# Kernel tuning notes

Measured on AMD Instinct MI355X. Metric: run time of the kernel, lower is better.

Reference implementation:

```python
import jax, jax.numpy as jnp
import numpy as np

N = 50000
E = 800000
D_IN = 128
D_H = 128
N_CLASSES = 40
N_HIDDEN = 2


def _gcn_norm(edge_index, num_nodes):
    # Add self loops, compute symmetric normalization D^-1/2 (A+I) D^-1/2
    loops = jnp.arange(num_nodes, dtype=edge_index.dtype)
    src = jnp.concatenate([edge_index[0], loops])
    dst = jnp.concatenate([edge_index[1], loops])
    deg = jax.ops.segment_sum(jnp.ones_like(src, dtype=jnp.float32), dst,
                              num_segments=num_nodes)
    dinv = jnp.where(deg > 0, jax.lax.rsqrt(jnp.maximum(deg, 1.0)), 0.0)
    norm = dinv[src] * dinv[dst]  # [E+N]
    return src, dst, norm


def _gcn_conv(x, src, dst, norm, W, b):
    h = x @ W                          # [N, d_out] transform first (PyG order)
    msg = h[src] * norm[:, None]       # gather + scale, [E+N, d_out]
    out = jax.ops.segment_sum(msg, dst, num_segments=x.shape[0])
    return out + b


def setup_inputs() -> dict:
    key = jax.random.key(0)
    ks = jax.random.split(key, 8)
    x = jax.random.normal(ks[0], (N, D_IN), dtype=jnp.float32)
    edge_index = jax.random.randint(ks[1], (2, E), 0, N, dtype=jnp.int64)
    s = 1.0 / np.sqrt(D_IN)
    W1 = jax.random.uniform(ks[2], (D_IN, D_H), minval=-s, maxval=s, dtype=jnp.float32)
    b1 = jnp.zeros((D_H,), dtype=jnp.float32)
    sh = 1.0 / np.sqrt(D_H)
    Wh = jax.random.uniform(ks[3], (N_HIDDEN, D_H, D_H), minval=-sh, maxval=sh, dtype=jnp.float32)
    bh = jnp.zeros((N_HIDDEN, D_H), dtype=jnp.float32)
    Wf = jax.random.uniform(ks[4], (D_H, N_CLASSES), minval=-sh, maxval=sh, dtype=jnp.float32)
    bf = jnp.zeros((N_CLASSES,), dtype=jnp.float32)
    return {"x": x, "edge_index": edge_index, "W1": W1, "b1": b1,
            "Wh": Wh, "bh": bh, "Wf": Wf, "bf": bf}


def reference(x, edge_index, W1, b1, Wh, bh, Wf, bf):
    src, dst, norm = _gcn_norm(edge_index, x.shape[0])
    h = jax.nn.relu(_gcn_conv(x, src, dst, norm, W1, b1))
    for i in range(Wh.shape[0]):  # small fixed layer count
        h = jax.nn.relu(_gcn_conv(h, src, dst, norm, Wh[i], bh[i]))
    # extra relu in original forward is a no-op after relu above
    return h @ Wf + bf
```

## Files before the change

kernel.cpp:

```cpp
#include <hip/hip_runtime.h>

#define D 128
#define NC 40

typedef __attribute__((ext_vector_type(8))) short short8v;
typedef __attribute__((ext_vector_type(4))) float f32x4;

__device__ __forceinline__ unsigned short f2bf(float f) {
    unsigned u = __float_as_uint(f);
    u += 0x7fff + ((u >> 16) & 1);
    return (unsigned short)(u >> 16);
}
__device__ __forceinline__ float bf2f(unsigned short h) {
    return __uint_as_float(((unsigned)h) << 16);
}

__device__ __forceinline__ int load_idx(const int* ei, long long pos, int is64) {
    return is64 ? ei[pos * 2] : ei[pos];
}

__device__ __forceinline__ int detect64(const int* __restrict__ ei) {
    int lane = threadIdx.x & 63;
    int hi = ei[lane * 2 + 1];
    return __any(hi != 0) ? 0 : 1;
}


__global__ void count_convert_kernel(const int* __restrict__ ei, int* __restrict__ deg,
                                     int E, int EB,
                                     const float* __restrict__ W1, const float* __restrict__ Wh,
                                     const float* __restrict__ Wf,
                                     unsigned short* __restrict__ Wc1, unsigned short* __restrict__ Wch0,
                                     unsigned short* __restrict__ Wch1, unsigned short* __restrict__ Wcf) {
    if (blockIdx.x < EB) {
        int is64 = detect64(ei);
        int e = blockIdx.x * 256 + threadIdx.x;
        if (e < E) {
            int d = load_idx(ei, (long long)E + e, is64);
            atomicAdd(&deg[d], 1);
        }
    } else {
        int idx = (blockIdx.x - EB) * 256 + threadIdx.x;
        if (idx < 49152) {
            int which = idx >> 14;
            int j = idx & 16383;
            int nn = j >> 7, k = j & 127;
            const float* W = (which == 0) ? W1 : (which == 1) ? Wh : Wh + 16384;
            unsigned short* o = (which == 0) ? Wc1 : (which == 1) ? Wch0 : Wch1;
            float v = W[k * 128 + nn];
            unsigned short h = f2bf(v);
            o[j] = h;
            o[16384 + j] = f2bf(v - bf2f(h));
        } else if (idx < 49152 + 6144) {
            int j = idx - 49152;
            int nn = j >> 7, k = j & 127;
            float v = (nn < NC) ? Wf[k * NC + nn] : 0.f;
            unsigned short h = f2bf(v);
            Wcf[j] = h;
            Wcf[6144 + j] = f2bf(v - bf2f(h));
        }
    }
}

__global__ void scan1_kernel(const int* __restrict__ deg, int* __restrict__ bsum, int m) {
    int i = blockIdx.x * 512 + threadIdx.x;
    int v = (i < m) ? deg[i] : 0;
    #pragma unroll
    for (int off = 32; off; off >>= 1) v += __shfl_down(v, off, 64);
    __shared__ int ws[8];
    if ((threadIdx.x & 63) == 0) ws[threadIdx.x >> 6] = v;
    __syncthreads();
    if (threadIdx.x == 0) {
        int s = 0;
        #pragma unroll
        for (int j = 0; j < 8; ++j) s += ws[j];
        bsum[blockIdx.x] = s;
    }
}

__global__ void scan3_kernel(const int* __restrict__ deg, const int* __restrict__ bsum,
                             int* __restrict__ rowptr, int* __restrict__ fill,
                             float* __restrict__ dinv, int n, int E, int nb) {
    int t = threadIdx.x;
    int lane = t & 63, w = t >> 6;
    int pv = (t < nb && t < (int)blockIdx.x) ? bsum[t] : 0;
    int rs = pv;
    #pragma unroll
    for (int off = 32; off; off >>= 1) rs += __shfl_down(rs, off, 64);
    __shared__ int red[8];
    if (lane == 0) red[w] = rs;
    __syncthreads();
    int base = 0;
    #pragma unroll
    for (int j = 0; j < 8; ++j) base += red[j];
    __syncthreads();

    int i = blockIdx.x * 512 + t;
    int v = (i < n) ? deg[i] : 0;
    int s = v;
    #pragma unroll
    for (int off = 1; off < 64; off <<= 1) {
        int x = __shfl_up(s, off, 64);
        if (lane >= off) s += x;
    }
    __shared__ int wsum[8];
    if (lane == 63) wsum[w] = s;
    __syncthreads();
    int wbase = 0;
    #pragma unroll
    for (int j = 0; j < 8; ++j) if (j < w) wbase += wsum[j];
    int excl = base + wbase + s - v;
    if (i < n) {
        rowptr[i] = excl;
        fill[i]   = excl;
        dinv[i]   = rsqrtf((float)(v + 1));
    }
    if (i == 0) rowptr[n] = E;
}

__global__ void scatter_kernel(const int* __restrict__ ei, int* __restrict__ fill,
                               const float* __restrict__ dinv, int2* __restrict__ col2, int E) {
    int is64 = detect64(ei);
    int e = blockIdx.x * 256 + threadIdx.x;
    if (e >= E) return;
    int s = load_idx(ei, (long long)e, is64);
    int d = load_idx(ei, (long long)E + e, is64);
    int pos = atomicAdd(&fill[d], 1);
    col2[pos] = make_int2(s, __float_as_int(dinv[s]));
}

__launch_bounds__(512)
__global__ void fused_layer_kernel(const float4* __restrict__ h4,
                                   const unsigned short* __restrict__ Wcvt,
                                   const float* __restrict__ bias,
                                   const float* __restrict__ dinv,
                                   const int* __restrict__ rowptr, const int2* __restrict__ col2,
                                   float* __restrict__ out, int n) {
    __shared__ unsigned short Ah[16 * 128];
    __shared__ unsigned short Al[16 * 128];
    int t = threadIdx.x;
    int g = t >> 5, l = t & 31;
    int node = blockIdx.x * 16 + g;
    int nd = (node < n) ? node : (n - 1);
    float dn = dinv[nd];
    size_t rowbase = (size_t)nd * 32;

    float4 hv = h4[rowbase + l];
    float4 acc;
    acc.x = hv.x * dn; acc.y = hv.y * dn; acc.z = hv.z * dn; acc.w = hv.w * dn;
    int e = rowptr[nd], e1 = rowptr[nd + 1];
    for (; e + 8 <= e1; e += 8) {
        int2 c[8];
        #pragma unroll
        for (int j = 0; j < 8; ++j) c[j] = col2[e + j];
        float4 v[8];
        #pragma unroll
        for (int j = 0; j < 8; ++j) v[j] = h4[(size_t)c[j].x * 32 + l];
        #pragma unroll
        for (int j = 0; j < 8; ++j) {
            float ds = __int_as_float(c[j].y);
            acc.x += v[j].x * ds; acc.y += v[j].y * ds;
            acc.z += v[j].z * ds; acc.w += v[j].w * ds;
        }
    }
    for (; e + 4 <= e1; e += 4) {
        int2 c[4];
        #pragma unroll
        for (int j = 0; j < 4; ++j) c[j] = col2[e + j];
        float4 v[4];
        #pragma unroll
        for (int j = 0; j < 4; ++j) v[j] = h4[(size_t)c[j].x * 32 + l];
        #pragma unroll
        for (int j = 0; j < 4; ++j) {
            float ds = __int_as_float(c[j].y);
            acc.x += v[j].x * ds; acc.y += v[j].y * ds;
            acc.z += v[j].z * ds; acc.w += v[j].w * ds;
        }
    }
    for (; e < e1; ++e) {
        int2 c = col2[e];
        float ds = __int_as_float(c.y);
        float4 v = h4[(size_t)c.x * 32 + l];
        acc.x += v.x * ds; acc.y += v.y * ds; acc.z += v.z * ds; acc.w += v.w * ds;
    }
    acc.x *= dn; acc.y *= dn; acc.z *= dn; acc.w *= dn;

    {
        ushort4 hi, lo;
        hi.x = f2bf(acc.x); lo.x = f2bf(acc.x - bf2f(hi.x));
        hi.y = f2bf(acc.y); lo.y = f2bf(acc.y - bf2f(hi.y));
        hi.z = f2bf(acc.z); lo.z = f2bf(acc.z - bf2f(hi.z));
        hi.w = f2bf(acc.w); lo.w = f2bf(acc.w - bf2f(hi.w));
        int off = (g << 8) + ((l << 3) ^ ((g & 7) << 4));
        *(ushort4*)((char*)Ah + off) = hi;
        *(ushort4*)((char*)Al + off) = lo;
    }
    __syncthreads();

    int l64 = t & 63, wv = t >> 6;
    int lr = l64 & 15, lh = l64 >> 4;
    int n0 = wv * 16;
    const unsigned short* Whi = Wcvt;
    const unsigned short* Wlo = Wcvt + 128 * 128;
    f32x4 o = (f32x4){0.f, 0.f, 0.f, 0.f};
    #pragma unroll
    for (int ks = 0; ks < 4; ++ks) {
        int aoff = (lr << 8) + (((ks << 6) + (lh << 4)) ^ ((lr & 7) << 4));
        short8v ah = *(short8v*)((char*)Ah + aoff);
        short8v al = *(short8v*)((char*)Al + aoff);
        int c0 = (n0 + lr) * 128 + ks * 32 + lh * 8;
        short8v bh = *(const short8v*)&Whi[c0];
        short8v bl = *(const short8v*)&Wlo[c0];
        o = __builtin_amdgcn_mfma_f32_16x16x32_bf16(ah, bh, o, 0, 0, 0);
        o = __builtin_amdgcn_mfma_f32_16x16x32_bf16(ah, bl, o, 0, 0, 0);
        o = __builtin_amdgcn_mfma_f32_16x16x32_bf16(al, bh, o, 0, 0, 0);
    }
    float bv = bias[n0 + lr];
    #pragma unroll
    for (int r = 0; r < 4; ++r) {
        int row = blockIdx.x * 16 + lh * 4 + r;
        if (row < n) out[(size_t)row * 128 + n0 + lr] = fmaxf(o[r] + bv, 0.f);
    }
}

__launch_bounds__(256)
__global__ void final_mfma_kernel(const float* __restrict__ A, const unsigned short* __restrict__ Wcvt,
                                  const float* __restrict__ bf, float* __restrict__ C, int M) {
    __shared__ unsigned short Ah[64 * 128];
    __shared__ unsigned short Al[64 * 128];
    int t = threadIdx.x;
    int l = t & 63, w = t >> 6;
    int lr = l & 15, lh = l >> 4;

    const unsigned short* Whi = Wcvt;
    const unsigned short* Wlo = Wcvt + 48 * 128;
    short8v bhi[3][4], blo[3][4];
    #pragma unroll
    for (int nt = 0; nt < 3; ++nt) {
        int n = nt * 16 + lr;
        #pragma unroll
        for (int ks = 0; ks < 4; ++ks) {
            bhi[nt][ks] = *(const short8v*)&Whi[n * 128 + ks * 32 + lh * 8];
            blo[nt][ks] = *(const short8v*)&Wlo[n * 128 + ks * 32 + lh * 8];
        }
    }

    int row0 = blockIdx.x * 64;
    #pragma unroll
    for (int c = 0; c < 4; ++c) {
        int chunk = c * 256 + t;
        int r  = chunk >> 4;
        int kc = chunk & 15;
        int gr = row0 + r; if (gr >= M) gr = M - 1;
        float4 a0 = *(const float4*)&A[(size_t)gr * 128 + kc * 8];
        float4 a1 = *(const float4*)&A[(size_t)gr * 128 + kc * 8 + 4];
        float av[8] = {a0.x, a0.y, a0.z, a0.w, a1.x, a1.y, a1.z, a1.w};
        short8v hv, lv;
        #pragma unroll
        for (int j = 0; j < 8; ++j) {
            unsigned short hi = f2bf(av[j]);
            hv[j] = (short)hi;
            lv[j] = (short)f2bf(av[j] - bf2f(hi));
        }
        int off = (r << 8) + ((kc << 4) ^ ((r & 7) << 4));
        *(short8v*)((char*)Ah + off) = hv;
        *(short8v*)((char*)Al + off) = lv;
    }
    __syncthreads();

    f32x4 acc[3];
    #pragma unroll
    for (int nt = 0; nt < 3; ++nt) acc[nt] = (f32x4){0.f, 0.f, 0.f, 0.f};
    int row = w * 16 + lr;
    #pragma unroll
    for (int ks = 0; ks < 4; ++ks) {
        int off = (row << 8) + (((ks << 6) + (lh << 4)) ^ ((row & 7) << 4));
        short8v ah = *(short8v*)((char*)Ah + off);
        short8v al = *(short8v*)((char*)Al + off);
        #pragma unroll
        for (int nt = 0; nt < 3; ++nt) {
            acc[nt] = __builtin_amdgcn_mfma_f32_16x16x32_bf16(ah, bhi[nt][ks], acc[nt], 0, 0, 0);
            acc[nt] = __builtin_amdgcn_mfma_f32_16x16x32_bf16(ah, blo[nt][ks], acc[nt], 0, 0, 0);
            acc[nt] = __builtin_amdgcn_mfma_f32_16x16x32_bf16(al, bhi[nt][ks], acc[nt], 0, 0, 0);
        }
    }
    #pragma unroll
    for (int nt = 0; nt < 3; ++nt) {
        int col = nt * 16 + lr;
        #pragma unroll
        for (int r = 0; r < 4; ++r) {
            int ro = row0 + w * 16 + lh * 4 + r;
            if (col < NC && ro < M) C[(size_t)ro * NC + col] = acc[nt][r] + bf[col];
        }
    }
}

extern "C" void kernel_launch(void* const* d_in, const int* in_sizes, int n_in,
                              void* d_out, int out_size, void* d_ws, size_t ws_size,
                              hipStream_t stream) {
    const float* x  = (const float*)d_in[0];
    const int*   ei = (const int*)d_in[1];
    const float* W1 = (const float*)d_in[2];
    const float* b1 = (const float*)d_in[3];
    const float* Wh = (const float*)d_in[4];
    const float* bh = (const float*)d_in[5];
    const float* Wf = (const float*)d_in[6];
    const float* bf = (const float*)d_in[7];
    float* out = (float*)d_out;

    int n = in_sizes[0] / D;
    int E = in_sizes[1] / 2;

    char* ws = (char*)d_ws;
    size_t off = 0;
    auto alloc = [&](size_t bytes) {
        void* p = ws + off;
        off = (off + bytes + 255) & ~(size_t)255;
        return p;
    };
    float* B0     = (float*)alloc((size_t)n * D * 4);
    float* B1     = (float*)alloc((size_t)n * D * 4);
    int*   deg    = (int*)alloc((size_t)n * 4);
    int*   rowptr = (int*)alloc((size_t)(n + 1) * 4);
    int*   fill   = (int*)alloc((size_t)n * 4);
    int2*  col2   = (int2*)alloc((size_t)E * 8);
    float* dinv   = (float*)alloc((size_t)n * 4);
    int*   bsum   = (int*)alloc(1024 * 4);
    unsigned short* Wc1  = (unsigned short*)alloc(2 * 128 * 128 * 2);
    unsigned short* Wch0 = (unsigned short*)alloc(2 * 128 * 128 * 2);
    unsigned short* Wch1 = (unsigned short*)alloc(2 * 128 * 128 * 2);
    unsigned short* Wcf  = (unsigned short*)alloc(2 * 48 * 128 * 2);

    int EB = (E + 255) / 256;
    int CB = (49152 + 6144 + 255) / 256;
    int nb = (n + 511) / 512;

    hipMemsetAsync(deg, 0, (size_t)n * 4, stream);
    count_convert_kernel<<<EB + CB, 256, 0, stream>>>(ei, deg, E, EB, W1, Wh, Wf, Wc1, Wch0, Wch1, Wcf);
    scan1_kernel<<<nb, 512, 0, stream>>>(deg, bsum, n);
    scan3_kernel<<<nb, 512, 0, stream>>>(deg, bsum, rowptr, fill, dinv, n, E, nb);
    scatter_kernel<<<EB, 256, 0, stream>>>(ei, fill, dinv, col2, E);

    int fgrid = (n + 15) / 16;

    fused_layer_kernel<<<fgrid, 512, 0, stream>>>((const float4*)x, Wc1, b1, dinv, rowptr, col2, B0, n);
    fused_layer_kernel<<<fgrid, 512, 0, stream>>>((const float4*)B0, Wch0, bh, dinv, rowptr, col2, B1, n);
    fused_layer_kernel<<<fgrid, 512, 0, stream>>>((const float4*)B1, Wch1, bh + D, dinv, rowptr, col2, B0, n);
    final_mfma_kernel<<<(n + 63) / 64, 256, 0, stream>>>(B0, Wcf, bf, out, n);
}
```

Baseline: 350.5 us.

## Sort nodes by degree bins to balance work in fused GCN layers

Builds a degree histogram during the scan, prefix-sums it, and creates a permutation grouping nodes with similar in-degree. The fused aggregation+MFMA layer kernel processes nodes in permuted order and writes outputs to the original rows via a shared index table. This aims to reduce divergence and tail imbalance among the 16 nodes in a block. In exchange it adds two small kernels, contended atomics on 64 bins, and non-sequential output and self-row accesses.

```diff
diff --git a/kernel.cpp b/kernel.cpp
--- a/kernel.cpp
+++ b/kernel.cpp
@@ -2,6 +2,7 @@
 
 #define D 128
 #define NC 40
+#define NBIN 64
 
 typedef __attribute__((ext_vector_type(8))) short short8v;
 typedef __attribute__((ext_vector_type(4))) float f32x4;
@@ -80,7 +81,8 @@
 
 __global__ void scan3_kernel(const int* __restrict__ deg, const int* __restrict__ bsum,
                              int* __restrict__ rowptr, int* __restrict__ fill,
-                             float* __restrict__ dinv, int n, int E, int nb) {
+                             float* __restrict__ dinv, int* __restrict__ hist,
+                             int n, int E, int nb) {
     int t = threadIdx.x;
     int lane = t & 63, w = t >> 6;
     int pv = (t < nb && t < (int)blockIdx.x) ? bsum[t] : 0;
@@ -114,8 +116,30 @@
         rowptr[i] = excl;
         fill[i]   = excl;
         dinv[i]   = rsqrtf((float)(v + 1));
+        atomicAdd(&hist[v < NBIN ? v : NBIN - 1], 1);
     }
     if (i == 0) rowptr[n] = E;
+}
+
+__global__ void binscan_kernel(const int* __restrict__ hist, int* __restrict__ cursor) {
+    int t = threadIdx.x;
+    int v = hist[t];
+    int s = v;
+    #pragma unroll
+    for (int off = 1; off < 64; off <<= 1) {
+        int x = __shfl_up(s, off, 64);
+        if (t >= off) s += x;
+    }
+    cursor[t] = s - v;
+}
+
+__global__ void permute_kernel(const int* __restrict__ deg, int* __restrict__ cursor,
+                               int* __restrict__ perm, int n) {
+    int i = blockIdx.x * 256 + threadIdx.x;
+    if (i >= n) return;
+    int v = deg[i];
+    int pos = atomicAdd(&cursor[v < NBIN ? v : NBIN - 1], 1);
+    perm[pos] = i;
 }
 
 __global__ void scatter_kernel(const int* __restrict__ ei, int* __restrict__ fill,
@@ -135,13 +159,16 @@
                                    const float* __restrict__ bias,
                                    const float* __restrict__ dinv,
                                    const int* __restrict__ rowptr, const int2* __restrict__ col2,
+                                   const int* __restrict__ perm,
                                    float* __restrict__ out, int n) {
     __shared__ unsigned short Ah[16 * 128];
     __shared__ unsigned short Al[16 * 128];
+    __shared__ int pnodes[16];
     int t = threadIdx.x;
     int g = t >> 5, l = t & 31;
-    int node = blockIdx.x * 16 + g;
-    int nd = (node < n) ? node : (n - 1);
+    int idx = blockIdx.x * 16 + g;
+    int nd = perm[(idx < n) ? idx : 0];
+    if (l == 0) pnodes[g] = (idx < n) ? nd : -1;
     float dn = dinv[nd];
     size_t rowbase = (size_t)nd * 32;
 
@@ -218,8 +245,8 @@
     float bv = bias[n0 + lr];
     #pragma unroll
     for (int r = 0; r < 4; ++r) {
-        int row = blockIdx.x * 16 + lh * 4 + r;
-        if (row < n) out[(size_t)row * 128 + n0 + lr] = fmaxf(o[r] + bv, 0.f);
+        int pr = pnodes[lh * 4 + r];
+        if (pr >= 0) out[(size_t)pr * 128 + n0 + lr] = fmaxf(o[r] + bv, 0.f);
     }
 }
 
@@ -326,6 +353,9 @@
     int2*  col2   = (int2*)alloc((size_t)E * 8);
     float* dinv   = (float*)alloc((size_t)n * 4);
     int*   bsum   = (int*)alloc(1024 * 4);
+    int*   hist   = (int*)alloc(NBIN * 4);
+    int*   cursor = (int*)alloc(NBIN * 4);
+    int*   perm   = (int*)alloc((size_t)n * 4);
     unsigned short* Wc1  = (unsigned short*)alloc(2 * 128 * 128 * 2);
     unsigned short* Wch0 = (unsigned short*)alloc(2 * 128 * 128 * 2);
     unsigned short* Wch1 = (unsigned short*)alloc(2 * 128 * 128 * 2);
@@ -336,15 +366,18 @@
     int nb = (n + 511) / 512;
 
     hipMemsetAsync(deg, 0, (size_t)n * 4, stream);
+    hipMemsetAsync(hist, 0, NBIN * 4, stream);
     count_convert_kernel<<<EB + CB, 256, 0, stream>>>(ei, deg, E, EB, W1, Wh, Wf, Wc1, Wch0, Wch1, Wcf);
     scan1_kernel<<<nb, 512, 0, stream>>>(deg, bsum, n);
-    scan3_kernel<<<nb, 512, 0, stream>>>(deg, bsum, rowptr, fill, dinv, n, E, nb);
+    scan3_kernel<<<nb, 512, 0, stream>>>(deg, bsum, rowptr, fill, dinv, hist, n, E, nb);
+    binscan_kernel<<<1, 64, 0, stream>>>(hist, cursor);
+    permute_kernel<<<(n + 255) / 256, 256, 0, stream>>>(deg, cursor, perm, n);
     scatter_kernel<<<EB, 256, 0, stream>>>(ei, fill, dinv, col2, E);
 
     int fgrid = (n + 15) / 16;
 
-    fused_layer_kernel<<<fgrid, 512, 0, stream>>>((const float4*)x, Wc1, b1, dinv, rowptr, col2, B0, n);
-    fused_layer_kernel<<<fgrid, 512, 0, stream>>>((const float4*)B0, Wch0, bh, dinv, rowptr, col2, B1, n);
-    fused_layer_kernel<<<fgrid, 512, 0, stream>>>((const float4*)B1, Wch1, bh + D, dinv, rowptr, col2, B0, n);
+    fused_layer_kernel<<<fgrid, 512, 0, stream>>>((const float4*)x, Wc1, b1, dinv, rowptr, col2, perm, B0, n);
+    fused_layer_kernel<<<fgrid, 512, 0, stream>>>((const float4*)B0, Wch0, bh, dinv, rowptr, col2, perm, B1, n);
+    fused_layer_kernel<<<fgrid, 512, 0, stream>>>((const float4*)B1, Wch1, bh + D, dinv, rowptr, col2, perm, B0, n);
     final_mfma_kernel<<<(n + 63) / 64, 256, 0, stream>>>(B0, Wcf, bf, out, n);
 }
```

Measured after the change: 592.0 us. 68.9% more time.

## Restructure GCN layer kernel to single-wave blocks handling 16 nodes

Applied to the files above, without the earlier changes.

Replaces the 512-thread fused aggregation+MFMA block with a 64-thread single-wave block that aggregates 16 nodes two at a time and builds MFMA A-fragments in registers via a small LDS staging buffer. The wave then computes all 8 output column tiles itself. This removes the block-wide barrier and large shared tiles, but cuts total waves eightfold, serialises the latency-bound neighbour gathers within each wave, and makes every wave reload the full weight matrix.

```diff
diff --git a/kernel.cpp b/kernel.cpp
--- a/kernel.cpp
+++ b/kernel.cpp
@@ -129,97 +129,115 @@
     col2[pos] = make_int2(s, __float_as_int(dinv[s]));
 }
 
-__launch_bounds__(512)
-__global__ void fused_layer_kernel(const float4* __restrict__ h4,
-                                   const unsigned short* __restrict__ Wcvt,
-                                   const float* __restrict__ bias,
-                                   const float* __restrict__ dinv,
-                                   const int* __restrict__ rowptr, const int2* __restrict__ col2,
-                                   float* __restrict__ out, int n) {
-    __shared__ unsigned short Ah[16 * 128];
-    __shared__ unsigned short Al[16 * 128];
-    int t = threadIdx.x;
-    int g = t >> 5, l = t & 31;
-    int node = blockIdx.x * 16 + g;
-    int nd = (node < n) ? node : (n - 1);
-    float dn = dinv[nd];
-    size_t rowbase = (size_t)nd * 32;
-
-    float4 hv = h4[rowbase + l];
-    float4 acc;
-    acc.x = hv.x * dn; acc.y = hv.y * dn; acc.z = hv.z * dn; acc.w = hv.w * dn;
-    int e = rowptr[nd], e1 = rowptr[nd + 1];
-    for (; e + 8 <= e1; e += 8) {
-        int2 c[8];
-        #pragma unroll
-        for (int j = 0; j < 8; ++j) c[j] = col2[e + j];
-        float4 v[8];
-        #pragma unroll
-        for (int j = 0; j < 8; ++j) v[j] = h4[(size_t)c[j].x * 32 + l];
-        #pragma unroll
-        for (int j = 0; j < 8; ++j) {
-            float ds = __int_as_float(c[j].y);
-            acc.x += v[j].x * ds; acc.y += v[j].y * ds;
-            acc.z += v[j].z * ds; acc.w += v[j].w * ds;
-        }
-    }
-    for (; e + 4 <= e1; e += 4) {
-        int2 c[4];
-        #pragma unroll
-        for (int j = 0; j < 4; ++j) c[j] = col2[e + j];
-        float4 v[4];
-        #pragma unroll
-        for (int j = 0; j < 4; ++j) v[j] = h4[(size_t)c[j].x * 32 + l];
-        #pragma unroll
-        for (int j = 0; j < 4; ++j) {
-            float ds = __int_as_float(c[j].y);
-            acc.x += v[j].x * ds; acc.y += v[j].y * ds;
-            acc.z += v[j].z * ds; acc.w += v[j].w * ds;
-        }
-    }
-    for (; e < e1; ++e) {
-        int2 c = col2[e];
-        float ds = __int_as_float(c.y);
-        float4 v = h4[(size_t)c.x * 32 + l];
-        acc.x += v.x * ds; acc.y += v.y * ds; acc.z += v.z * ds; acc.w += v.w * ds;
-    }
-    acc.x *= dn; acc.y *= dn; acc.z *= dn; acc.w *= dn;
-
-    {
+__launch_bounds__(64)
+__global__ void fused_wave_kernel(const float4* __restrict__ h4,
+                                  const unsigned short* __restrict__ Wcvt,
+                                  const float* __restrict__ bias,
+                                  const float* __restrict__ dinv,
+                                  const int* __restrict__ rowptr, const int2* __restrict__ col2,
+                                  float* __restrict__ out, int n) {
+    __shared__ unsigned short S[2][2][128];
+    int l = threadIdx.x & 63;
+    int p = l >> 5, li = l & 31;
+    int kg = l >> 4, lr = l & 15;
+    int base = blockIdx.x * 16;
+    if (base >= n) return;
+
+    short8v fAh[4], fAl[4];
+    #pragma unroll
+    for (int ks = 0; ks < 4; ++ks) {
+        fAh[ks] = (short8v){0,0,0,0,0,0,0,0};
+        fAl[ks] = (short8v){0,0,0,0,0,0,0,0};
+    }
+
+    for (int j = 0; j < 8; ++j) {
+        int node = base + 2 * j + p;
+        int nd = (node < n) ? node : (n - 1);
+        float dn = dinv[nd];
+        size_t rowbase = (size_t)nd * 32;
+        float4 hv = h4[rowbase + li];
+        float4 acc;
+        acc.x = hv.x * dn; acc.y = hv.y * dn; acc.z = hv.z * dn; acc.w = hv.w * dn;
+        int e = rowptr[nd], e1 = rowptr[nd + 1];
+        for (; e + 8 <= e1; e += 8) {
+            int2 c[8];
+            #pragma unroll
+            for (int q = 0; q < 8; ++q) c[q] = col2[e + q];
+            float4 v[8];
+            #pragma unroll
+            for (int q = 0; q < 8; ++q) v[q] = h4[(size_t)c[q].x * 32 + li];
+            #pragma unroll
+            for (int q = 0; q < 8; ++q) {
+                float ds = __int_as_float(c[q].y);
+                acc.x += v[q].x * ds; acc.y += v[q].y * ds;
+                acc.z += v[q].z * ds; acc.w += v[q].w * ds;
+            }
+        }
+        for (; e + 4 <= e1; e += 4) {
+            int2 c[4];
+            #pragma unroll
+            for (int q = 0; q < 4; ++q) c[q] = col2[e + q];
+            float4 v[4];
+            #pragma unroll
+            for (int q = 0; q < 4; ++q) v[q] = h4[(size_t)c[q].x * 32 + li];
+            #pragma unroll
+            for (int q = 0; q < 4; ++q) {
+                float ds = __int_as_float(c[q].y);
+                acc.x += v[q].x * ds; acc.y += v[q].y * ds;
+                acc.z += v[q].z * ds; acc.w += v[q].w * ds;
+            }
+        }
+        for (; e < e1; ++e) {
+            int2 c = col2[e];
+            float ds = __int_as_float(c.y);
+            float4 v = h4[(size_t)c.x * 32 + li];
+            acc.x += v.x * ds; acc.y += v.y * ds; acc.z += v.z * ds; acc.w += v.w * ds;
+        }
+        acc.x *= dn; acc.y *= dn; acc.z *= dn; acc.w *= dn;
+
         ushort4 hi, lo;
         hi.x = f2bf(acc.x); lo.x = f2bf(acc.x - bf2f(hi.x));
         hi.y = f2bf(acc.y); lo.y = f2bf(acc.y - bf2f(hi.y));
         hi.z = f2bf(acc.z); lo.z = f2bf(acc.z - bf2f(hi.z));
         hi.w = f2bf(acc.w); lo.w = f2bf(acc.w - bf2f(hi.w));
-        int off = (g << 8) + ((l << 3) ^ ((g & 7) << 4));
-        *(ushort4*)((char*)Ah + off) = hi;
-        *(ushort4*)((char*)Al + off) = lo;
-    }
-    __syncthreads();
-
-    int l64 = t & 63, wv = t >> 6;
-    int lr = l64 & 15, lh = l64 >> 4;
-    int n0 = wv * 16;
+        *(ushort4*)&S[0][p][li * 4] = hi;
+        *(ushort4*)&S[1][p][li * 4] = lo;
+        __builtin_amdgcn_wave_barrier();
+        if ((lr >> 1) == j) {
+            int rp = lr & 1;
+            #pragma unroll
+            for (int ks = 0; ks < 4; ++ks) {
+                fAh[ks] = *(short8v*)&S[0][rp][ks * 32 + kg * 8];
+                fAl[ks] = *(short8v*)&S[1][rp][ks * 32 + kg * 8];
+            }
+        }
+        __builtin_amdgcn_wave_barrier();
+    }
+
     const unsigned short* Whi = Wcvt;
     const unsigned short* Wlo = Wcvt + 128 * 128;
-    f32x4 o = (f32x4){0.f, 0.f, 0.f, 0.f};
-    #pragma unroll
-    for (int ks = 0; ks < 4; ++ks) {
-        int aoff = (lr << 8) + (((ks << 6) + (lh << 4)) ^ ((lr & 7) << 4));
-        short8v ah = *(short8v*)((char*)Ah + aoff);
-        short8v al = *(short8v*)((char*)Al + aoff);
-        int c0 = (n0 + lr) * 128 + ks * 32 + lh * 8;
-        short8v bh = *(const short8v*)&Whi[c0];
-        short8v bl = *(const short8v*)&Wlo[c0];
-        o = __builtin_amdgcn_mfma_f32_16x16x32_bf16(ah, bh, o, 0, 0, 0);
-        o = __builtin_amdgcn_mfma_f32_16x16x32_bf16(ah, bl, o, 0, 0, 0);
-        o = __builtin_amdgcn_mfma_f32_16x16x32_bf16(al, bh, o, 0, 0, 0);
-    }
-    float bv = bias[n0 + lr];
-    #pragma unroll
-    for (int r = 0; r < 4; ++r) {
-        int row = blockIdx.x * 16 + lh * 4 + r;
-        if (row < n) out[(size_t)row * 128 + n0 + lr] = fmaxf(o[r] + bv, 0.f);
+    #pragma unroll
+    for (int nt = 0; nt < 8; ++nt) {
+        int col = nt * 16 + lr;
+        short8v bh[4], bl[4];
+        #pragma unroll
+        for (int ks = 0; ks < 4; ++ks) {
+            bh[ks] = *(const short8v*)&Whi[col * 128 + ks * 32 + kg * 8];
+            bl[ks] = *(const short8v*)&Wlo[col * 128 + ks * 32 + kg * 8];
+        }
+        f32x4 o = (f32x4){0.f, 0.f, 0.f, 0.f};
+        #pragma unroll
+        for (int ks = 0; ks < 4; ++ks) {
+            o = __builtin_amdgcn_mfma_f32_16x16x32_bf16(fAh[ks], bh[ks], o, 0, 0, 0);
+            o = __builtin_amdgcn_mfma_f32_16x16x32_bf16(fAh[ks], bl[ks], o, 0, 0, 0);
+            o = __builtin_amdgcn_mfma_f32_16x16x32_bf16(fAl[ks], bh[ks], o, 0, 0, 0);
+        }
+        float bv = bias[col];
+        #pragma unroll
+        for (int r = 0; r < 4; ++r) {
+            int row = base + kg * 4 + r;
+            if (row < n) out[(size_t)row * 128 + col] = fmaxf(o[r] + bv, 0.f);
+        }
     }
 }
 
@@ -343,8 +361,8 @@
 
     int fgrid = (n + 15) / 16;
 
-    fused_layer_kernel<<<fgrid, 512, 0, stream>>>((const float4*)x, Wc1, b1, dinv, rowptr, col2, B0, n);
-    fused_layer_kernel<<<fgrid, 512, 0, stream>>>((const float4*)B0, Wch0, bh, dinv, rowptr, col2, B1, n);
-    fused_layer_kernel<<<fgrid, 512, 0, stream>>>((const float4*)B1, Wch1, bh + D, dinv, rowptr, col2, B0, n);
+    fused_wave_kernel<<<fgrid, 64, 0, stream>>>((const float4*)x, Wc1, b1, dinv, rowptr, col2, B0, n);
+    fused_wave_kernel<<<fgrid, 64, 0, stream>>>((const float4*)B0, Wch0, bh, dinv, rowptr, col2, B1, n);
+    fused_wave_kernel<<<fgrid, 64, 0, stream>>>((const float4*)B1, Wch1, bh + D, dinv, rowptr, col2, B0, n);
     final_mfma_kernel<<<(n + 63) / 64, 256, 0, stream>>>(B0, Wcf, bf, out, n);
 }
```

New measurement: 349.6 us. About the same (-0.3%).
